# Kernel optimization log

Measured on AMD Instinct MI355X. Metric: run time of the kernel, lower is better.

Reference implementation:

```python
import jax, jax.numpy as jnp
import numpy as np
from jax import lax
import math

SCALES = (128.0, 256.0, 512.0)
ASPECT_RATIOS = (0.5, 1.0, 2.0)
NMS_THR = 0.7
PRENMS_TOPK = 2000   # rpn_train_prenms_topk (module is in training mode at __init__)
POST_TOPK = 300      # rpn_train_topk
MIN_SIZE = 16.0      # rpn_min_size
BBOX_CLAMP = math.log(1000.0 / 16.0)


def conv2d(x, w, b, pad):
    y = lax.conv_general_dilated(x, w, (1, 1), pad,
                                 dimension_numbers=('NCHW', 'OIHW', 'NCHW'))
    return y + b[None, :, None, None]


def generate_anchors(img_h, img_w, grid_h, grid_w, dtype=jnp.float32):
    # Mirrors RegionProposalNetwork.generate_anchors
    stride_h = img_h // grid_h
    stride_w = img_w // grid_w
    scales = jnp.asarray(SCALES, dtype)
    ratios = jnp.asarray(ASPECT_RATIOS, dtype)
    h = jnp.sqrt(ratios)
    w = 1.0 / h
    ws = (w[:, None] * scales[None, :]).reshape(-1)   # (K,)
    hs = (h[:, None] * scales[None, :]).reshape(-1)
    base = jnp.round(jnp.stack([-ws, -hs, ws, hs], axis=1) / 2.0)  # (K,4)
    sx = jnp.arange(grid_w, dtype=dtype) * stride_w
    sy = jnp.arange(grid_h, dtype=dtype) * stride_h
    syy, sxx = jnp.meshgrid(sy, sx, indexing='ij')
    sxx = sxx.reshape(-1); syy = syy.reshape(-1)
    shifts = jnp.stack([sxx, syy, sxx, syy], axis=1)               # (HW,4)
    anchors = (shifts[:, None, :] + base[None, :, :]).reshape(-1, 4)  # (HW*K,4)
    return anchors


def decode(deltas, anchors):
    wa = anchors[:, 2] - anchors[:, 0]
    ha = anchors[:, 3] - anchors[:, 1]
    cxa = anchors[:, 0] + 0.5 * wa
    cya = anchors[:, 1] + 0.5 * ha
    dx, dy = deltas[..., 0], deltas[..., 1]
    dw = jnp.minimum(deltas[..., 2], BBOX_CLAMP)
    dh = jnp.minimum(deltas[..., 3], BBOX_CLAMP)
    cx = dx * wa + cxa
    cy = dy * ha + cya
    w = jnp.exp(dw) * wa
    h = jnp.exp(dh) * ha
    return jnp.stack([cx - 0.5 * w, cy - 0.5 * h, cx + 0.5 * w, cy + 0.5 * h], axis=-1)


def pairwise_iou(a, b):
    area_a = (a[:, 2] - a[:, 0]) * (a[:, 3] - a[:, 1])
    area_b = (b[:, 2] - b[:, 0]) * (b[:, 3] - b[:, 1])
    lt = jnp.maximum(a[:, None, :2], b[None, :, :2])
    rb = jnp.minimum(a[:, None, 2:], b[None, :, 2:])
    wh = jnp.clip(rb - lt, 0.0)
    inter = wh[..., 0] * wh[..., 1]
    return inter / (area_a[:, None] + area_b[None, :] - inter)


def nms_keep(boxes, init_suppressed):
    # boxes are already sorted by descending score; O(N^2) matrix NMS.
    iou = lax.stop_gradient(pairwise_iou(boxes, boxes))
    n = boxes.shape[0]
    idxs = jnp.arange(n)
    def body(i, st):
        keep, sup = st
        valid = jnp.logical_not(sup[i])
        keep = keep.at[i].set(valid)
        sup = sup | (valid & (iou[i] > NMS_THR) & (idxs > i))
        return keep, sup
    keep, _ = lax.fori_loop(0, n, body,
                            (jnp.zeros(n, dtype=bool), init_suppressed))
    return keep


def filter_one(proposals, scores, img_h, img_w):
    # pre-NMS top-k
    sc, idx = lax.top_k(scores, PRENMS_TOPK)
    boxes = proposals[idx]
    # clip to image
    x1 = jnp.clip(boxes[:, 0], 0.0, img_w)
    y1 = jnp.clip(boxes[:, 1], 0.0, img_h)
    x2 = jnp.clip(boxes[:, 2], 0.0, img_w)
    y2 = jnp.clip(boxes[:, 3], 0.0, img_h)
    boxes = jnp.stack([x1, y1, x2, y2], axis=1)
    # min-size filter (masked, fixed shape)
    small = ((x2 - x1) < MIN_SIZE) | ((y2 - y1) < MIN_SIZE)
    sc = jnp.where(small, -jnp.inf, sc)
    # NMS then post-NMS top-k
    keep = nms_keep(boxes, small)
    post = jnp.where(keep, sc, -jnp.inf)
    fs, fi = lax.top_k(post, POST_TOPK)
    return boxes[fi], fs


def setup_inputs() -> dict:
    key = jax.random.key(0)
    ks = jax.random.split(key, 8)
    B, C, H, W, IMG, K = 4, 512, 64, 64, 1024, 9
    image = jax.random.normal(ks[0], (B, 3, IMG, IMG), jnp.float32)
    feature_map = jax.random.normal(ks[1], (B, C, H, W), jnp.float32)
    # init: normal(std=0.01) weights, zero bias
    w_conv = 0.01 * jax.random.normal(ks[2], (C, C, 3, 3), jnp.float32)
    b_conv = jnp.zeros((C,), jnp.float32)
    w_cls = 0.01 * jax.random.normal(ks[3], (K, C, 1, 1), jnp.float32)
    b_cls = jnp.zeros((K,), jnp.float32)
    w_box = 0.01 * jax.random.normal(ks[4], (4 * K, C, 1, 1), jnp.float32)
    b_box = jnp.zeros((4 * K,), jnp.float32)
    return {"image": image, "feature_map": feature_map,
            "w_conv": w_conv, "b_conv": b_conv,
            "w_cls": w_cls, "b_cls": b_cls,
            "w_box": w_box, "b_box": b_box}


def reference(image, feature_map, w_conv, b_conv, w_cls, b_cls, w_box, b_box):
    B, _, img_h, img_w = image.shape
    _, _, gh, gw = feature_map.shape
    feat = jax.nn.relu(conv2d(feature_map, w_conv, b_conv, 'SAME'))
    cls = conv2d(feat, w_cls, b_cls, 'VALID')   # (B, K, H, W)
    box = conv2d(feat, w_box, b_box, 'VALID')   # (B, 4K, H, W)
    scores = jax.nn.sigmoid(cls.transpose(0, 2, 3, 1).reshape(B, -1))   # (B, N)
    deltas = box.transpose(0, 2, 3, 1).reshape(B, -1, 4)                # (B, N, 4)
    anchors = generate_anchors(img_h, img_w, gh, gw)                    # (N, 4)
    proposals = decode(deltas, anchors)                                 # (B, N, 4)
    props, sc = jax.vmap(lambda p, s: filter_one(p, s, float(img_h), float(img_w)))(proposals, scores)
    return props, sc   # (B, POST_TOPK, 4), (B, POST_TOPK)
```

## Files before the change

### kernel.cpp

```cpp
#include <hip/hip_runtime.h>
#include <math.h>

typedef unsigned long long U64;
typedef _Float16 half8 __attribute__((ext_vector_type(8)));
typedef float f32x16 __attribute__((ext_vector_type(16)));

__device__ const float g_bw[9] = {91.f, 181.f, 362.f, 64.f, 128.f, 256.f, 45.f, 91.f, 181.f};
__device__ const float g_bh[9] = {45.f, 91.f, 181.f, 64.f, 128.f, 256.f, 91.f, 181.f, 362.f};

__device__ inline f32x16 zero16() {
    f32x16 z;
#pragma unroll
    for (int i = 0; i < 16; ++i) z[i] = 0.f;
    return z;
}

#define GLOAD16(G, L)                                                  \
    __builtin_amdgcn_global_load_lds(                                  \
        (const __attribute__((address_space(1))) void*)(G),            \
        (__attribute__((address_space(3))) void*)(L), 16, 0, 0)

__global__ __launch_bounds__(256) void k_prep_fm(const float* __restrict__ fm,
                                                 _Float16* __restrict__ fpi) {
    __shared__ float tile[64][65];
    int cg = blockIdx.x, h = blockIdx.y, b = blockIdx.z;
    int t = threadIdx.x;
    int cl = t >> 2, w0 = (t & 3) * 16;
    const float* src = fm + (((size_t)(b * 512 + cg * 64 + cl) * 64 + h) * 64 + w0);
#pragma unroll
    for (int l = 0; l < 4; ++l) {
        float4 v = *(const float4*)(src + l * 4);
        tile[cl][w0 + l * 4 + 0] = v.x; tile[cl][w0 + l * 4 + 1] = v.y;
        tile[cl][w0 + l * 4 + 2] = v.z; tile[cl][w0 + l * 4 + 3] = v.w;
    }
    __syncthreads();
    int w = t & 63, pth = t >> 6;
    int chunkrel = pth >> 1, half = pth & 1;
    _Float16* dst = fpi + ((size_t)((b * 66 + h + 1) * 66) + (w + 1)) * 1024 +
                    (cg * 2 + chunkrel) * 64 + half * 32;
#pragma unroll
    for (int g8 = 0; g8 < 4; ++g8) {
        half8 v;
#pragma unroll
        for (int i = 0; i < 8; ++i) {
            float x = tile[chunkrel * 32 + g8 * 8 + i][w];
            _Float16 hi = (_Float16)x;
            v[i] = half ? (_Float16)((x - (float)hi) * 2048.0f) : hi;
        }
        *(half8*)(dst + g8 * 8) = v;
    }
}

__global__ __launch_bounds__(256) void k_prep_w(const float* __restrict__ w_conv,
                                                _Float16* __restrict__ wki) {
    __shared__ float wb[4608];
    int o = blockIdx.x, t = threadIdx.x;
    for (int e = t; e < 4608; e += 256) wb[e] = w_conv[(size_t)o * 4608 + e];
    __syncthreads();
    for (int e = t; e < 9216; e += 256) {
        int s = e & 63, chunk = e >> 6;
        int tap = chunk >> 4, cgi = chunk & 15;
        int c = cgi * 32 + (s & 31);
        float x = wb[c * 9 + tap];
        _Float16 hi = (_Float16)x;
        wki[(size_t)o * 9216 + e] = (s < 32) ? hi : (_Float16)((x - (float)hi) * 2048.0f);
    }
}

__global__ __launch_bounds__(256, 2) void k_conv_mfma(
    const _Float16* __restrict__ fpi, const _Float16* __restrict__ wki,
    const float* __restrict__ bconv, float* __restrict__ feat) {
    __shared__ _Float16 As[2][128][64];
    __shared__ _Float16 Bs[2][128][64];
    const int t = threadIdx.x;
    const int lane = t & 63, wv = t >> 6;
    const int wm = wv >> 1, wn = wv & 1;
    int flat = (int)blockIdx.x + 128 * (int)blockIdx.y;
    int fid = (flat & 7) * 64 + (flat >> 3);
    const int p0 = (fid >> 2) * 128, o0 = (fid & 3) * 128;

    const char* baseA[4];
    const char* baseB[4];
#pragma unroll
    for (int q = 0; q < 4; ++q) {
        int row = wv * 32 + q * 8 + (lane >> 3);
        int qs = (lane & 7) ^ (row & 7);
        int P = p0 + row;
        int bb = P >> 12, hh = (P >> 6) & 63, ww = P & 63;
        baseA[q] = (const char*)fpi + ((size_t)((bb * 66 + hh) * 66 + ww)) * 2048 + qs * 16;
        baseB[q] = (const char*)wki + (size_t)(o0 + row) * 18432 + qs * 16;
    }

    f32x16 acc0[2][2], acc1[2][2];
#pragma unroll
    for (int mi = 0; mi < 2; ++mi)
#pragma unroll
        for (int ni = 0; ni < 2; ++ni) { acc0[mi][ni] = zero16(); acc1[mi][ni] = zero16(); }

    auto issue = [&](int it2, int buf) {
        int tap = it2 >> 4;
        int ry = (tap * 11) >> 5, rx = tap - ry * 3;
        int ka = (ry * 66 + rx) * 2048 + (it2 & 15) * 128;
        int kb = it2 * 128;
#pragma unroll
        for (int q = 0; q < 4; ++q) {
            GLOAD16(baseA[q] + ka, &As[buf][wv * 32 + q * 8][0]);
            GLOAD16(baseB[q] + kb, &Bs[buf][wv * 32 + q * 8][0]);
        }
    };

    issue(0, 0);
    issue(1, 1);

    for (int it = 0; it < 144; ++it) {
        int cur = it & 1;
        if (it < 143) { asm volatile("s_waitcnt vmcnt(8)" ::: "memory"); }
        else          { asm volatile("s_waitcnt vmcnt(0)" ::: "memory"); }
        __builtin_amdgcn_s_barrier();
        __builtin_amdgcn_sched_barrier(0);

        const char* ab = (const char*)As + cur * 16384;
        const char* bb2 = (const char*)Bs + cur * 16384;
        half8 af[2][2][2], bf[2][2][2];
        const int lg = (lane >> 5) * 16;
#pragma unroll
        for (int mi = 0; mi < 2; ++mi) {
            int rA = wm * 64 + mi * 32 + (lane & 31);
            int xa = (rA & 7) << 4, ba = rA * 128;
#pragma unroll
            for (int hl = 0; hl < 2; ++hl)
#pragma unroll
                for (int kh = 0; kh < 2; ++kh)
                    af[mi][hl][kh] = *(const half8*)(ab + ba + ((hl * 64 + kh * 32 + lg) ^ xa));
        }
#pragma unroll
        for (int ni = 0; ni < 2; ++ni) {
            int rB = wn * 64 + ni * 32 + (lane & 31);
            int xb = (rB & 7) << 4, bb0 = rB * 128;
#pragma unroll
            for (int hl = 0; hl < 2; ++hl)
#pragma unroll
                for (int kh = 0; kh < 2; ++kh)
                    bf[ni][hl][kh] = *(const half8*)(bb2 + bb0 + ((hl * 64 + kh * 32 + lg) ^ xb));
        }
#pragma unroll
        for (int mi = 0; mi < 2; ++mi)
#pragma unroll
            for (int ni = 0; ni < 2; ++ni) {
                acc0[mi][ni] = __builtin_amdgcn_mfma_f32_32x32x16_f16(af[mi][0][0], bf[ni][0][0], acc0[mi][ni], 0, 0, 0);
                acc0[mi][ni] = __builtin_amdgcn_mfma_f32_32x32x16_f16(af[mi][0][1], bf[ni][0][1], acc0[mi][ni], 0, 0, 0);
                acc1[mi][ni] = __builtin_amdgcn_mfma_f32_32x32x16_f16(af[mi][0][0], bf[ni][1][0], acc1[mi][ni], 0, 0, 0);
                acc1[mi][ni] = __builtin_amdgcn_mfma_f32_32x32x16_f16(af[mi][0][1], bf[ni][1][1], acc1[mi][ni], 0, 0, 0);
                acc1[mi][ni] = __builtin_amdgcn_mfma_f32_32x32x16_f16(af[mi][1][0], bf[ni][0][0], acc1[mi][ni], 0, 0, 0);
                acc1[mi][ni] = __builtin_amdgcn_mfma_f32_32x32x16_f16(af[mi][1][1], bf[ni][0][1], acc1[mi][ni], 0, 0, 0);
            }

        __builtin_amdgcn_sched_barrier(0);
        __builtin_amdgcn_s_barrier();
        __builtin_amdgcn_sched_barrier(0);
        if (it < 142) issue(it + 2, cur);
    }

#pragma unroll
    for (int mi = 0; mi < 2; ++mi)
#pragma unroll
        for (int ni = 0; ni < 2; ++ni) {
            int col = o0 + wn * 64 + ni * 32 + (lane & 31);
            float bv = bconv[col];
            int rbase = p0 + wm * 64 + mi * 32 + 4 * (lane >> 5);
#pragma unroll
            for (int q = 0; q < 16; ++q) {
                int row = rbase + (q & 3) + 8 * (q >> 2);
                float v = acc0[mi][ni][q] + acc1[mi][ni][q] * 4.8828125e-4f + bv;
                feat[(size_t)row * 512 + col] = fmaxf(v, 0.f);
            }
        }
}

__global__ __launch_bounds__(256) void k_heads(const float* __restrict__ feat,
                                               const float* __restrict__ w_cls,
                                               const float* __restrict__ b_cls,
                                               const float* __restrict__ w_box,
                                               const float* __restrict__ b_box,
                                               U64* __restrict__ keys,
                                               float4* __restrict__ proposals) {
    __shared__ float red[3][64][45];
    int t = threadIdx.x;
    int px = t & 63, cq = t >> 6;
    int p = blockIdx.x * 64 + px;
    const float* fr = feat + (size_t)p * 512 + cq * 128;
    float acc[45];
#pragma unroll
    for (int o = 0; o < 45; ++o) acc[o] = 0.f;
    for (int c = 0; c < 128; c += 4) {
        float4 f = *(const float4*)(fr + c);
#pragma unroll
        for (int o = 0; o < 45; ++o) {
            const float* wr = ((o < 9) ? (w_cls + o * 512) : (w_box + (o - 9) * 512)) + cq * 128 + c;
            acc[o] += f.x * wr[0] + f.y * wr[1] + f.z * wr[2] + f.w * wr[3];
        }
    }
    if (cq > 0) {
#pragma unroll
        for (int o = 0; o < 45; ++o) red[cq - 1][px][o] = acc[o];
    }
    __syncthreads();
    if (cq == 0) {
#pragma unroll
        for (int o = 0; o < 45; ++o) acc[o] += red[0][px][o] + red[1][px][o] + red[2][px][o];
        int b = p >> 12, pixloc = p & 4095;
        int h = pixloc >> 6, w = pixloc & 63;
        int ibase = b * 36864 + pixloc * 9;
#pragma unroll
        for (int a = 0; a < 9; ++a) {
            float logit = acc[a] + b_cls[a];
            float s = 1.f / (1.f + expf(-logit));
            keys[ibase + a] = (((U64)(__float_as_uint(s) ^ 0x80000000u)) << 32) |
                              (unsigned)(~(unsigned)(pixloc * 9 + a));
            float dx = acc[9 + a * 4 + 0] + b_box[a * 4 + 0];
            float dy = acc[9 + a * 4 + 1] + b_box[a * 4 + 1];
            float dw = fminf(acc[9 + a * 4 + 2] + b_box[a * 4 + 2], 4.135166556742356f);
            float dh = fminf(acc[9 + a * 4 + 3] + b_box[a * 4 + 3], 4.135166556742356f);
            float wa = 2.f * g_bw[a], ha = 2.f * g_bh[a];
            float cx = dx * wa + (float)(w * 16);
            float cy = dy * ha + (float)(h * 16);
            float pw = expf(dw) * wa;
            float ph = expf(dh) * ha;
            proposals[ibase + a] =
                make_float4(cx - 0.5f * pw, cy - 0.5f * ph, cx + 0.5f * pw, cy + 0.5f * ph);
        }
    }
}

__device__ inline void cmp_stage(U64* s, int j, int k, int tid) {
    for (int p = tid; p < 1024; p += 256) {
        int il = ((p & ~(j - 1)) << 1) | (p & (j - 1));
        int ip = il | j;
        U64 a = s[il], c = s[ip];
        bool desc = ((il & k) == 0);
        bool sw = desc ? (a < c) : (a > c);
        if (sw) { s[il] = c; s[ip] = a; }
    }
}

__global__ __launch_bounds__(256) void k_sort_chunk(const U64* __restrict__ keys,
                                                    U64* __restrict__ run) {
    __shared__ U64 s[2048];
    int b = blockIdx.x / 18, ch = blockIdx.x % 18;
    int tid = threadIdx.x;
    const U64* src = keys + (size_t)b * 36864 + ch * 2048;
    for (int e = tid; e < 2048; e += 256) s[e] = src[e];
    __syncthreads();
    for (int k = 2; k <= 2048; k <<= 1)
        for (int j = k >> 1; j >= 1; j >>= 1) {
            cmp_stage(s, j, k, tid);
            __syncthreads();
        }
    U64* dst = run + ((size_t)b * 18 + ch) * 2048;
    for (int e = tid; e < 2048; e += 256) dst[e] = s[e];
}

__global__ __launch_bounds__(256) void k_merge4(const U64* __restrict__ in,
                                                U64* __restrict__ out, int nc) {
    __shared__ U64 s[4096];
    int g = blockIdx.x, b = blockIdx.y;
    int tid = threadIdx.x;
    int r0 = g * 4;
    int n = nc - r0; if (n > 4) n = 4;
    const U64* base = in + (size_t)b * 18 * 2048;
    U64* O = out + ((size_t)b * 18 + g) * 2048;
    for (int e = tid; e < 2048; e += 256) s[e] = base[(size_t)r0 * 2048 + e];
    for (int m = 1; m < n; ++m) {
        for (int e = tid; e < 2048; e += 256) s[4095 - e] = base[(size_t)(r0 + m) * 2048 + e];
        __syncthreads();
        for (int e = tid; e < 2048; e += 256) {
            U64 a = s[e], c = s[e + 2048];
            s[e] = (a >= c) ? a : c;
        }
        __syncthreads();
        for (int j = 1024; j >= 1; j >>= 1) {
            for (int p = tid; p < 1024; p += 256) {
                int il = ((p & ~(j - 1)) << 1) | (p & (j - 1));
                int ip = il | j;
                U64 a = s[il], c = s[ip];
                if (a < c) { s[il] = c; s[ip] = a; }
            }
            __syncthreads();
        }
    }
    for (int e = tid; e < 2048; e += 256) O[e] = s[e];
}

__global__ __launch_bounds__(256) void k_topk_gather(const U64* __restrict__ runf,
                                                     const float4* __restrict__ proposals,
                                                     float4* __restrict__ tb_boxes,
                                                     float* __restrict__ tb_scores) {
    int g = blockIdx.x * 256 + threadIdx.x;
    if (g >= 8000) return;
    int b = g / 2000, r = g - b * 2000;
    U64 key = runf[(size_t)b * 18 * 2048 + r];
    unsigned n = ~((unsigned)key);
    float s = __uint_as_float(((unsigned)(key >> 32)) ^ 0x80000000u);
    float4 p = proposals[b * 36864 + (int)n];
    float x1 = fminf(fmaxf(p.x, 0.f), 1024.f);
    float y1 = fminf(fmaxf(p.y, 0.f), 1024.f);
    float x2 = fminf(fmaxf(p.z, 0.f), 1024.f);
    float y2 = fminf(fmaxf(p.w, 0.f), 1024.f);
    bool small_ = ((x2 - x1) < 16.f) || ((y2 - y1) < 16.f);
    tb_boxes[g] = make_float4(x1, y1, x2, y2);
    tb_scores[g] = small_ ? -INFINITY : s;
}

__global__ __launch_bounds__(64) void k_nms_mask(const float4* __restrict__ tb_boxes,
                                                 U64* __restrict__ mask) {
    int jt = blockIdx.x, it = blockIdx.y, b = blockIdx.z;
    int tid = threadIdx.x;
    __shared__ float4 jb[64];
    int j0 = jt * 64;
    {
        int j = j0 + tid;
        jb[tid] = (j < 2000) ? tb_boxes[b * 2000 + j] : make_float4(0.f, 0.f, 0.f, 0.f);
    }
    __syncthreads();
    int i = it * 64 + tid;
    if (i >= 2000) return;
    float4 bi = tb_boxes[b * 2000 + i];
    float ai = (bi.z - bi.x) * (bi.w - bi.y);
    U64 bits = 0;
#pragma unroll 4
    for (int jj = 0; jj < 64; ++jj) {
        int j = j0 + jj;
        float4 bj = jb[jj];
        float aj = (bj.z - bj.x) * (bj.w - bj.y);
        float ltx = fmaxf(bi.x, bj.x), lty = fmaxf(bi.y, bj.y);
        float rbx = fminf(bi.z, bj.z), rby = fminf(bi.w, bj.w);
        float ww = fmaxf(rbx - ltx, 0.f), hh2 = fmaxf(rby - lty, 0.f);
        float inter = ww * hh2;
        float iou = inter / (ai + aj - inter);
        if ((j > i) && (j < 2000) && (iou > 0.7f)) bits |= (1ull << jj);
    }
    mask[((size_t)b * 2000 + i) * 32 + jt] = bits;
}

__global__ __launch_bounds__(64) void k_nms_scan(const float4* __restrict__ tb_boxes,
                                                 const float* __restrict__ tb_scores,
                                                 const U64* __restrict__ mask,
                                                 float* __restrict__ out) {
    int b = blockIdx.x;
    int lane = threadIdx.x;
    __shared__ U64 mbuf[2][2048];
    __shared__ unsigned short keeplist[2000];
    __shared__ unsigned char keepflag[2000];
    __shared__ unsigned short fillq[304];

    U64 remv = 0;
    if (lane < 32) {
        for (int jj = 0; jj < 64; ++jj) {
            int j = (lane << 6) | jj;
            if (j < 2000 && tb_scores[b * 2000 + j] == -INFINITY) remv |= (1ull << jj);
        }
    }
    const U64* mb = mask + (size_t)b * 2000 * 32;
#pragma unroll
    for (int q = 0; q < 32; ++q) {
        int e = q * 64 + lane;
        mbuf[0][e] = mb[(e >> 5) * 32 + (e & 31)];
    }
    __syncthreads();

    int nkeep = 0;
    for (int ch = 0; ch < 32; ++ch) {
        int cur = ch & 1;
        U64 v[32];
        if (ch < 31) {
#pragma unroll
            for (int q = 0; q < 32; ++q) {
                int e = q * 64 + lane;
                int row = (ch + 1) * 64 + (e >> 5), wd = e & 31;
                v[q] = (row < 2000) ? mb[(size_t)row * 32 + wd] : 0ull;
            }
        }
        int iend = min(64, 2000 - ch * 64);
        U64 w_all = __shfl(remv, ch);
        for (int ii = 0; ii < iend; ++ii) {
            bool sup = (w_all >> ii) & 1ull;
            int i = ch * 64 + ii;
            if (!sup) {
                if (lane == 0) keeplist[nkeep] = (unsigned short)i;
                U64 mrow = mbuf[cur][(ii << 5) | (lane & 31)];
                if (lane < 32) remv |= mrow;
                w_all |= mbuf[cur][(ii << 5) | ch];
                nkeep++;
            }
            if (lane == 0) keepflag[i] = sup ? (unsigned char)0 : (unsigned char)1;
        }
        if (ch < 31) {
#pragma unroll
            for (int q = 0; q < 32; ++q) mbuf[cur ^ 1][q * 64 + lane] = v[q];
        }
        __syncthreads();
    }

    if (lane == 0) {
        int need = 300 - nkeep, c = 0;
        for (int i = 0; i < 2000 && c < need; ++i)
            if (!keepflag[i]) fillq[c++] = (unsigned short)i;
    }
    __syncthreads();
    for (int r = lane; r < 300; r += 64) {
        int src; float sc;
        if (r < nkeep) { src = keeplist[r]; sc = tb_scores[b * 2000 + src]; }
        else           { src = fillq[r - nkeep]; sc = -INFINITY; }
        float4 bx = tb_boxes[b * 2000 + src];
        int ob = (b * 300 + r) * 4;
        out[ob + 0] = bx.x; out[ob + 1] = bx.y; out[ob + 2] = bx.z; out[ob + 3] = bx.w;
        out[4800 + b * 300 + r] = sc;
    }
}

extern "C" void kernel_launch(void* const* d_in, const int* in_sizes, int n_in,
                              void* d_out, int out_size, void* d_ws, size_t ws_size,
                              hipStream_t stream) {
    (void)in_sizes; (void)n_in; (void)out_size; (void)ws_size;
    const float* feature_map = (const float*)d_in[1];
    const float* w_conv = (const float*)d_in[2];
    const float* b_conv = (const float*)d_in[3];
    const float* w_cls  = (const float*)d_in[4];
    const float* b_cls  = (const float*)d_in[5];
    const float* w_box  = (const float*)d_in[6];
    const float* b_box  = (const float*)d_in[7];
    float* out = (float*)d_out;

    char* ws = (char*)d_ws;
    size_t off = 0;
    auto alloc = [&](size_t bytes) {
        void* p = ws + off;
        off = (off + bytes + 255) & ~(size_t)255;
        return p;
    };
    const size_t fpi_elems = 4ull * 66 * 66 * 1024;
    _Float16* fpi = (_Float16*)alloc(fpi_elems * 2);
    _Float16* wki = (_Float16*)alloc(512ull * 9216 * 2);
    float*  feat      = (float*) alloc(16384ull * 512 * 4);
    float4* proposals = (float4*)alloc(4ull * 36864 * 16);
    U64*    keys      = (U64*)   alloc(4ull * 36864 * 8);
    U64*    run0      = (U64*)   alloc(4ull * 18 * 2048 * 8);
    U64*    run1      = (U64*)   alloc(4ull * 18 * 2048 * 8);
    float4* tb_boxes  = (float4*)alloc(8000ull * 16);
    float*  tb_scores = (float*) alloc(8000ull * 4);
    U64*    nmsmask   = (U64*)   alloc(8000ull * 32 * 8);

    hipMemsetAsync(fpi, 0, fpi_elems * 2, stream);
    k_prep_fm<<<dim3(8, 64, 4), 256, 0, stream>>>(feature_map, fpi);
    k_prep_w<<<512, 256, 0, stream>>>(w_conv, wki);
    k_conv_mfma<<<dim3(128, 4), 256, 0, stream>>>(fpi, wki, b_conv, feat);
    k_heads<<<256, 256, 0, stream>>>(feat, w_cls, b_cls, w_box, b_box, keys, proposals);

    k_sort_chunk<<<72, 256, 0, stream>>>(keys, run0);
    k_merge4<<<dim3(5, 4), 256, 0, stream>>>(run0, run1, 18);
    k_merge4<<<dim3(2, 4), 256, 0, stream>>>(run1, run0, 5);
    k_merge4<<<dim3(1, 4), 256, 0, stream>>>(run0, run1, 2);

    k_topk_gather<<<32, 256, 0, stream>>>(run1, proposals, tb_boxes, tb_scores);
    k_nms_mask<<<dim3(32, 32, 4), 64, 0, stream>>>(tb_boxes, nmsmask);
    k_nms_scan<<<4, 64, 0, stream>>>(tb_boxes, tb_scores, nmsmask, out);
}
```

Baseline: 786.8 us.

## Zero only padding border in prep, interleave MFMA with LDS loads, register-resident NMS scan

```diff
diff --git a/kernel.cpp b/kernel.cpp
--- a/kernel.cpp
+++ b/kernel.cpp
@@ -22,9 +22,20 @@
 
 __global__ __launch_bounds__(256) void k_prep_fm(const float* __restrict__ fm,
                                                  _Float16* __restrict__ fpi) {
+    int bid = blockIdx.x, b = blockIdx.y;
+    int t = threadIdx.x;
+    if (bid >= 512) {
+        int ci = bid - 512;
+        int hp, wp;
+        if (ci < 66)       { hp = 0;  wp = ci; }
+        else if (ci < 132) { hp = 65; wp = ci - 66; }
+        else { int k = ci - 132; hp = 1 + (k & 63); wp = (k < 64) ? 0 : 65; }
+        uint2 z; z.x = 0u; z.y = 0u;
+        *(uint2*)(fpi + ((size_t)(b * 66 + hp) * 66 + wp) * 1024 + t * 4) = z;
+        return;
+    }
     __shared__ float tile[64][65];
-    int cg = blockIdx.x, h = blockIdx.y, b = blockIdx.z;
-    int t = threadIdx.x;
+    int cg = bid & 7, h = bid >> 3;
     int cl = t >> 2, w0 = (t & 3) * 16;
     const float* src = fm + (((size_t)(b * 512 + cg * 64 + cl) * 64 + h) * 64 + w0);
 #pragma unroll
@@ -112,6 +123,32 @@
     issue(0, 0);
     issue(1, 1);
 
+#define LOADA(mi_)                                                              \
+    {                                                                           \
+        int rA = wm * 64 + (mi_) * 32 + (lane & 31);                            \
+        int xa = (rA & 7) << 4, ba = rA * 128;                                  \
+        af[mi_][0][0] = *(const half8*)(ab + ba + ((0 + lg) ^ xa));             \
+        af[mi_][0][1] = *(const half8*)(ab + ba + ((32 + lg) ^ xa));            \
+        af[mi_][1][0] = *(const half8*)(ab + ba + ((64 + lg) ^ xa));            \
+        af[mi_][1][1] = *(const half8*)(ab + ba + ((96 + lg) ^ xa));            \
+    }
+#define LOADB(ni_)                                                              \
+    {                                                                           \
+        int rB = wn * 64 + (ni_) * 32 + (lane & 31);                            \
+        int xb = (rB & 7) << 4, bb0 = rB * 128;                                 \
+        bf[ni_][0][0] = *(const half8*)(bb2 + bb0 + ((0 + lg) ^ xb));           \
+        bf[ni_][0][1] = *(const half8*)(bb2 + bb0 + ((32 + lg) ^ xb));          \
+        bf[ni_][1][0] = *(const half8*)(bb2 + bb0 + ((64 + lg) ^ xb));          \
+        bf[ni_][1][1] = *(const half8*)(bb2 + bb0 + ((96 + lg) ^ xb));          \
+    }
+#define QUAD(mi_, ni_)                                                                                     \
+    acc0[mi_][ni_] = __builtin_amdgcn_mfma_f32_32x32x16_f16(af[mi_][0][0], bf[ni_][0][0], acc0[mi_][ni_], 0, 0, 0); \
+    acc0[mi_][ni_] = __builtin_amdgcn_mfma_f32_32x32x16_f16(af[mi_][0][1], bf[ni_][0][1], acc0[mi_][ni_], 0, 0, 0); \
+    acc1[mi_][ni_] = __builtin_amdgcn_mfma_f32_32x32x16_f16(af[mi_][0][0], bf[ni_][1][0], acc1[mi_][ni_], 0, 0, 0); \
+    acc1[mi_][ni_] = __builtin_amdgcn_mfma_f32_32x32x16_f16(af[mi_][0][1], bf[ni_][1][1], acc1[mi_][ni_], 0, 0, 0); \
+    acc1[mi_][ni_] = __builtin_amdgcn_mfma_f32_32x32x16_f16(af[mi_][1][0], bf[ni_][0][0], acc1[mi_][ni_], 0, 0, 0); \
+    acc1[mi_][ni_] = __builtin_amdgcn_mfma_f32_32x32x16_f16(af[mi_][1][1], bf[ni_][0][1], acc1[mi_][ni_], 0, 0, 0);
+
     for (int it = 0; it < 144; ++it) {
         int cur = it & 1;
         if (it < 143) { asm volatile("s_waitcnt vmcnt(8)" ::: "memory"); }
@@ -121,39 +158,22 @@
 
         const char* ab = (const char*)As + cur * 16384;
         const char* bb2 = (const char*)Bs + cur * 16384;
+        const int lg = (lane >> 5) * 16;
         half8 af[2][2][2], bf[2][2][2];
-        const int lg = (lane >> 5) * 16;
-#pragma unroll
-        for (int mi = 0; mi < 2; ++mi) {
-            int rA = wm * 64 + mi * 32 + (lane & 31);
-            int xa = (rA & 7) << 4, ba = rA * 128;
-#pragma unroll
-            for (int hl = 0; hl < 2; ++hl)
-#pragma unroll
-                for (int kh = 0; kh < 2; ++kh)
-                    af[mi][hl][kh] = *(const half8*)(ab + ba + ((hl * 64 + kh * 32 + lg) ^ xa));
-        }
-#pragma unroll
-        for (int ni = 0; ni < 2; ++ni) {
-            int rB = wn * 64 + ni * 32 + (lane & 31);
-            int xb = (rB & 7) << 4, bb0 = rB * 128;
-#pragma unroll
-            for (int hl = 0; hl < 2; ++hl)
-#pragma unroll
-                for (int kh = 0; kh < 2; ++kh)
-                    bf[ni][hl][kh] = *(const half8*)(bb2 + bb0 + ((hl * 64 + kh * 32 + lg) ^ xb));
-        }
-#pragma unroll
-        for (int mi = 0; mi < 2; ++mi)
-#pragma unroll
-            for (int ni = 0; ni < 2; ++ni) {
-                acc0[mi][ni] = __builtin_amdgcn_mfma_f32_32x32x16_f16(af[mi][0][0], bf[ni][0][0], acc0[mi][ni], 0, 0, 0);
-                acc0[mi][ni] = __builtin_amdgcn_mfma_f32_32x32x16_f16(af[mi][0][1], bf[ni][0][1], acc0[mi][ni], 0, 0, 0);
-                acc1[mi][ni] = __builtin_amdgcn_mfma_f32_32x32x16_f16(af[mi][0][0], bf[ni][1][0], acc1[mi][ni], 0, 0, 0);
-                acc1[mi][ni] = __builtin_amdgcn_mfma_f32_32x32x16_f16(af[mi][0][1], bf[ni][1][1], acc1[mi][ni], 0, 0, 0);
-                acc1[mi][ni] = __builtin_amdgcn_mfma_f32_32x32x16_f16(af[mi][1][0], bf[ni][0][0], acc1[mi][ni], 0, 0, 0);
-                acc1[mi][ni] = __builtin_amdgcn_mfma_f32_32x32x16_f16(af[mi][1][1], bf[ni][0][1], acc1[mi][ni], 0, 0, 0);
-            }
+
+        LOADA(0) LOADB(0) LOADA(1)
+        __builtin_amdgcn_s_setprio(1);
+        QUAD(0, 0)
+        __builtin_amdgcn_s_setprio(0);
+        LOADB(1)
+        __builtin_amdgcn_s_setprio(1);
+        QUAD(1, 0) QUAD(0, 1) QUAD(1, 1)
+        __builtin_amdgcn_s_setprio(0);
+
+        __builtin_amdgcn_sched_group_barrier(0x100, 12, 0);
+        __builtin_amdgcn_sched_group_barrier(0x008, 6, 0);
+        __builtin_amdgcn_sched_group_barrier(0x100, 4, 0);
+        __builtin_amdgcn_sched_group_barrier(0x008, 18, 0);
 
         __builtin_amdgcn_sched_barrier(0);
         __builtin_amdgcn_s_barrier();
@@ -348,7 +368,6 @@
                                                  float* __restrict__ out) {
     int b = blockIdx.x;
     int lane = threadIdx.x;
-    __shared__ U64 mbuf[2][2048];
     __shared__ unsigned short keeplist[2000];
     __shared__ unsigned char keepflag[2000];
     __shared__ unsigned short fillq[304];
@@ -361,45 +380,46 @@
         }
     }
     const U64* mb = mask + (size_t)b * 2000 * 32;
-#pragma unroll
-    for (int q = 0; q < 32; ++q) {
-        int e = q * 64 + lane;
-        mbuf[0][e] = mb[(e >> 5) * 32 + (e & 31)];
-    }
-    __syncthreads();
-
+
+    U64 cva[32], cvb[32];
     int nkeep = 0;
-    for (int ch = 0; ch < 32; ++ch) {
-        int cur = ch & 1;
-        U64 v[32];
-        if (ch < 31) {
-#pragma unroll
-            for (int q = 0; q < 32; ++q) {
-                int e = q * 64 + lane;
-                int row = (ch + 1) * 64 + (e >> 5), wd = e & 31;
-                v[q] = (row < 2000) ? mb[(size_t)row * 32 + wd] : 0ull;
+
+    auto loadchunk = [&](U64 (&cv)[32], int ch) {
+#pragma unroll
+        for (int q = 0; q < 32; ++q) {
+            int row = ch * 64 + q * 2 + (lane >> 5), wd = lane & 31;
+            cv[q] = (row < 2000) ? mb[(size_t)row * 32 + wd] : 0ull;
+        }
+    };
+    auto process = [&](U64 (&cv)[32], int ch) {
+        int base = ch * 64;
+        int iend = (2000 - base < 64) ? (2000 - base) : 64;
+        U64 w_all = __shfl(remv, ch);
+#pragma unroll
+        for (int ii = 0; ii < 64; ++ii) {
+            if (ii < iend) {
+                bool sup = (w_all >> ii) & 1ull;
+                int i = base + ii;
+                if (!sup) {
+                    if (lane == 0) keeplist[nkeep] = (unsigned short)i;
+                    U64 mrow = __shfl(cv[ii >> 1], ((ii & 1) << 5) | (lane & 31));
+                    if (lane < 32) remv |= mrow;
+                    w_all |= __shfl(cv[ii >> 1], ((ii & 1) << 5) | ch);
+                    nkeep++;
+                }
+                if (lane == 0) keepflag[i] = sup ? (unsigned char)0 : (unsigned char)1;
             }
         }
-        int iend = min(64, 2000 - ch * 64);
-        U64 w_all = __shfl(remv, ch);
-        for (int ii = 0; ii < iend; ++ii) {
-            bool sup = (w_all >> ii) & 1ull;
-            int i = ch * 64 + ii;
-            if (!sup) {
-                if (lane == 0) keeplist[nkeep] = (unsigned short)i;
-                U64 mrow = mbuf[cur][(ii << 5) | (lane & 31)];
-                if (lane < 32) remv |= mrow;
-                w_all |= mbuf[cur][(ii << 5) | ch];
-                nkeep++;
-            }
-            if (lane == 0) keepflag[i] = sup ? (unsigned char)0 : (unsigned char)1;
-        }
-        if (ch < 31) {
-#pragma unroll
-            for (int q = 0; q < 32; ++q) mbuf[cur ^ 1][q * 64 + lane] = v[q];
-        }
-        __syncthreads();
-    }
+    };
+
+    loadchunk(cva, 0);
+    for (int ch2 = 0; ch2 < 32; ch2 += 2) {
+        loadchunk(cvb, ch2 + 1);
+        process(cva, ch2);
+        if (ch2 + 2 < 32) loadchunk(cva, ch2 + 2);
+        process(cvb, ch2 + 1);
+    }
+    __syncthreads();
 
     if (lane == 0) {
         int need = 300 - nkeep, c = 0;
@@ -450,8 +470,7 @@
     float*  tb_scores = (float*) alloc(8000ull * 4);
     U64*    nmsmask   = (U64*)   alloc(8000ull * 32 * 8);
 
-    hipMemsetAsync(fpi, 0, fpi_elems * 2, stream);
-    k_prep_fm<<<dim3(8, 64, 4), 256, 0, stream>>>(feature_map, fpi);
+    k_prep_fm<<<dim3(772, 4), 256, 0, stream>>>(feature_map, fpi);
     k_prep_w<<<512, 256, 0, stream>>>(w_conv, wki);
     k_conv_mfma<<<dim3(128, 4), 256, 0, stream>>>(fpi, wki, b_conv, feat);
     k_heads<<<256, 256, 0, stream>>>(feat, w_cls, b_cls, w_box, b_box, keys, proposals);
```

New measurement: 760.3 us. 1.03x faster.
